# Kernel tuning notes

Hardware: AMD Instinct MI355X
Metric: run time of the kernel (lower is better)

## Reference

```python
import jax, jax.numpy as jnp
import numpy as np

B, N, K, M = 4, 32768, 128, 1024
C_IN, C_OUT, C_ATT, H = 256, 256, 256, 8
G = 32  # GroupNorm groups
EPS = 1e-6


def heat_diffusion(x, mass, evals, evecs, t):
    # to_basis: evecs^T @ (mass * x)  -> [B,K,C]
    x_spec = jnp.einsum('bnk,bnc->bkc', evecs, x * mass[..., None])
    coefs = jnp.exp(-evals[..., None] * t[None, None, :])  # [B,K,C]
    # from_basis: evecs @ spec -> [B,N,C]
    return jnp.einsum('bnk,bkc->bnc', evecs, coefs * x_spec)


def setup_inputs() -> dict:
    key = jax.random.key(0)
    ks = jax.random.split(key, 16)
    x = jax.random.normal(ks[0], (B, N, C_IN), jnp.float32)
    mass = jax.random.uniform(ks[1], (B, N), jnp.float32, 0.1, 1.0)
    evals = jnp.sort(jax.random.uniform(ks[2], (B, K), jnp.float32, 0.0, 10.0), axis=-1)
    evecs = jax.random.normal(ks[3], (B, N, K), jnp.float32) / np.sqrt(N)
    # unique sorted farthest-point indices per mesh (equiv. to boolean mask with M True)
    far_idx = jnp.stack([jnp.sort(jax.random.permutation(jax.random.fold_in(ks[4], b), N)[:M])
                         for b in range(B)]).astype(jnp.int32)
    s = 1.0 / np.sqrt(C_IN)
    params = dict(
        diff_in_t=jnp.full((C_IN,), 0.01, jnp.float32),
        diff_out_t=jnp.full((C_OUT,), 0.01, jnp.float32),
        gn_w=jnp.ones((C_IN,), jnp.float32),
        gn_b=jnp.zeros((C_IN,), jnp.float32),
        Wq=jax.random.normal(ks[5], (C_IN, C_ATT), jnp.float32) * s,
        bq=jnp.zeros((C_ATT,), jnp.float32),
        Wk=jax.random.normal(ks[6], (C_IN, C_ATT), jnp.float32) * s,
        bk=jnp.zeros((C_ATT,), jnp.float32),
        Wv=jax.random.normal(ks[7], (C_IN, C_ATT), jnp.float32) * s,
        bv=jnp.zeros((C_ATT,), jnp.float32),
        Wo=jax.random.normal(ks[8], (C_ATT, C_OUT), jnp.float32) * s,
        bo=jnp.zeros((C_OUT,), jnp.float32),
        out_w=jnp.ones((C_OUT,), jnp.float32),
    )
    return dict(x=x, mass=mass, evals=evals, evecs=evecs, far_idx=far_idx, **params)


def reference(x, mass, evals, evecs, far_idx, diff_in_t, diff_out_t, gn_w, gn_b,
              Wq, bq, Wk, bk, Wv, bv, Wo, bo, out_w):
    # clamp (torch does this in-place under no_grad)
    diff_in_t = jnp.maximum(diff_in_t, 1e-8)
    diff_out_t = jnp.maximum(diff_out_t, 1e-8)
    out_w = jnp.maximum(out_w, 1e-8)

    x = heat_diffusion(x, mass, evals, evecs, diff_in_t)  # [B,N,C_IN]

    # masked gather of farthest points -> [B,M,C_IN]
    x_far = jnp.take_along_axis(x, far_idx[..., None], axis=1)

    # GroupNorm over (group-channels, points)
    xg = x_far.reshape(B, M, G, C_IN // G)
    mu = jnp.mean(xg, axis=(1, 3), keepdims=True)
    var = jnp.var(xg, axis=(1, 3), keepdims=True)
    xg = (xg - mu) * jax.lax.rsqrt(var + EPS)
    x_far = xg.reshape(B, M, C_IN) * gn_w + gn_b

    d = C_ATT // H
    q = (x_far @ Wq + bq).reshape(B, M, H, d)
    k = (x_far @ Wk + bk).reshape(B, M, H, d)
    v = (x_far @ Wv + bv).reshape(B, M, H, d)
    scores = jnp.einsum('bqhd,bkhd->bhqk', q, k) / np.sqrt(d)
    attn = jax.nn.softmax(scores, axis=-1)
    x_far = jnp.einsum('bhqk,bkhd->bqhd', attn, v).reshape(B, M, C_ATT)
    x_far = x_far @ Wo + bo  # [B,M,C_OUT]

    # scatter back into zeros at the farthest-point rows
    z = jnp.zeros((B, N, C_OUT), x.dtype)
    z = z.at[jnp.arange(B)[:, None], far_idx].set(x_far)

    out = heat_diffusion(z, mass, evals, evecs, diff_out_t)
    return out * out_w[None, None, :]
```

## Files before the change

### kernel.cpp

```cpp
#include <hip/hip_runtime.h>
#include <hip/hip_bf16.h>


#define Bn 4
#define Nn 32768
#define Kn 128
#define Cn 256
#define Mn 1024
#define Hn 8
#define Dn 32
#define NCH 64
#define MCH 16

typedef _Float16 f16;
typedef _Float16 f16x8 __attribute__((ext_vector_type(8)));
typedef float f32x4 __attribute__((ext_vector_type(4)));
typedef unsigned int u32;
typedef unsigned int u32x4 __attribute__((ext_vector_type(4)));

__device__ __forceinline__ void gload_lds16(const float* g, float* l) {
    __builtin_amdgcn_global_load_lds(
        (const __attribute__((address_space(1))) void*)g,
        (__attribute__((address_space(3))) void*)l, 16, 0, 0);
}

static __device__ __forceinline__ u32 packf16(f16 a, f16 b) {
    union { f16 h[2]; u32 u; } x;
    x.h[0] = a; x.h[1] = b;
    return x.u;
}

__global__ __launch_bounds__(512) void k_tobasis1(
    const float* __restrict__ x, const float* __restrict__ mass,
    const float* __restrict__ evecs, float* __restrict__ part)
{
    const int nch = blockIdx.x, b = blockIdx.z;
    const int n0 = nch * (Nn / NCH);
    const int t = threadIdx.x;
    const int lane = t & 63, w = t >> 6;
    const int lr = lane & 15, lg = lane >> 4;
    const int wm = (w & 1) * 64;
    const int wc = (w >> 1) * 64;

    __shared__ __align__(16) float evS[2][32][128];
    __shared__ __align__(16) float xS[2][32][256];
    __shared__ __align__(16) f16 evT[128][64];
    __shared__ __align__(16) f16 xT[256][64];
    __shared__ __align__(16) float massS[512];

    const size_t rb0 = (size_t)b * Nn + n0;
    const float* ebase = evecs + rb0 * Kn;
    const float* xbase = x + rb0 * Cn;

    f32x4 acc[4][4] = {};

    if (w < 2) gload_lds16(mass + rb0 + w * 256 + lane * 4, massS + w * 256);
#pragma unroll
    for (int ss = 0; ss < 2; ss++) {
        const float* eb = ebase + (size_t)ss * 32 * Kn;
        const float* xb = xbase + (size_t)ss * 32 * Cn;
#pragma unroll
        for (int iw = 0; iw < 2; iw++)
            gload_lds16(eb + (w * 2 + iw) * 256 + lane * 4, &evS[ss][0][0] + (w * 2 + iw) * 256);
#pragma unroll
        for (int iw = 0; iw < 4; iw++)
            gload_lds16(xb + (w * 4 + iw) * 256 + lane * 4, &xS[ss][0][0] + (w * 4 + iw) * 256);
    }

    for (int s = 0; s < 16; s++) {
        const int p = s & 1;
        if (s == 15) { asm volatile("s_waitcnt vmcnt(0)" ::: "memory"); }
        else         { asm volatile("s_waitcnt vmcnt(6)" ::: "memory"); }
        __builtin_amdgcn_sched_barrier(0);
        __builtin_amdgcn_s_barrier();

        {
            const int k = t & 127;
            const int g = t >> 7;
            f16x8 hv, lv;
#pragma unroll
            for (int r = 0; r < 8; r++) {
                const float f = evS[p][g * 8 + r][k];
                const f16 h = (f16)f;
                hv[r] = h;
                lv[r] = (f16)(f - (float)h);
            }
            *(f16x8*)&evT[k][((g) ^ (k & 7)) * 8] = hv;
            *(f16x8*)&evT[k][((4 + g) ^ (k & 7)) * 8] = lv;
        }
        {
            const int c = t & 255;
            const int g2 = t >> 8;
#pragma unroll
            for (int jj = 0; jj < 2; jj++) {
                const int ch = g2 * 2 + jj;
                f16x8 hv, lv;
#pragma unroll
                for (int r = 0; r < 8; r++) {
                    const int n = ch * 8 + r;
                    const float f = xS[p][n][c] * massS[s * 32 + n];
                    const f16 h = (f16)f;
                    hv[r] = h;
                    lv[r] = (f16)(f - (float)h);
                }
                *(f16x8*)&xT[c][((ch) ^ (c & 7)) * 8] = hv;
                *(f16x8*)&xT[c][((4 + ch) ^ (c & 7)) * 8] = lv;
            }
        }

        asm volatile("s_waitcnt lgkmcnt(0)" ::: "memory");
        __builtin_amdgcn_sched_barrier(0);
        __builtin_amdgcn_s_barrier();

        if (s + 2 < 16) {
            const float* eb = ebase + (size_t)(s + 2) * 32 * Kn;
            const float* xb = xbase + (size_t)(s + 2) * 32 * Cn;
#pragma unroll
            for (int iw = 0; iw < 2; iw++)
                gload_lds16(eb + (w * 2 + iw) * 256 + lane * 4, &evS[p][0][0] + (w * 2 + iw) * 256);
#pragma unroll
            for (int iw = 0; iw < 4; iw++)
                gload_lds16(xb + (w * 4 + iw) * 256 + lane * 4, &xS[p][0][0] + (w * 4 + iw) * 256);
        }

        f16x8 aH[4], aL[4], bH[4], bL[4];
#pragma unroll
        for (int i = 0; i < 4; i++) {
            const int rk = wm + i * 16 + lr;
            aH[i] = *(const f16x8*)&evT[rk][((lg) ^ (rk & 7)) * 8];
            aL[i] = *(const f16x8*)&evT[rk][((4 + lg) ^ (rk & 7)) * 8];
            const int rc = wc + i * 16 + lr;
            bH[i] = *(const f16x8*)&xT[rc][((lg) ^ (rc & 7)) * 8];
            bL[i] = *(const f16x8*)&xT[rc][((4 + lg) ^ (rc & 7)) * 8];
        }
#pragma unroll
        for (int i = 0; i < 4; i++)
#pragma unroll
            for (int j = 0; j < 4; j++) {
                acc[i][j] = __builtin_amdgcn_mfma_f32_16x16x32_f16(aH[i], bH[j], acc[i][j], 0, 0, 0);
                acc[i][j] = __builtin_amdgcn_mfma_f32_16x16x32_f16(aH[i], bL[j], acc[i][j], 0, 0, 0);
                acc[i][j] = __builtin_amdgcn_mfma_f32_16x16x32_f16(aL[i], bH[j], acc[i][j], 0, 0, 0);
            }
    }

    float* dst = part + ((size_t)b * NCH + nch) * (Kn * Cn);
#pragma unroll
    for (int i = 0; i < 4; i++)
#pragma unroll
        for (int j = 0; j < 4; j++) {
            const int m0 = wm + i * 16 + lg * 4;
            const int c = wc + j * 16 + lr;
#pragma unroll
            for (int r = 0; r < 4; r++)
                dst[(size_t)(m0 + r) * Cn + c] = acc[i][j][r];
        }
}

__global__ __launch_bounds__(256) void k_reduce(
    const float* __restrict__ part, int nchunks,
    const float* __restrict__ evals, const float* __restrict__ tvec,
    float* __restrict__ spec)
{
    const int b = blockIdx.x >> 7, k = blockIdx.x & 127, c = threadIdx.x;
    float ssum = 0.f;
    const float* p = part + ((size_t)b * nchunks * Kn + k) * Cn + c;
    for (int j = 0; j < nchunks; j++) ssum += p[(size_t)j * Kn * Cn];
    const float lam = evals[b * Kn + k];
    const float tt = fmaxf(tvec[c], 1e-8f);
    spec[((size_t)b * Kn + k) * Cn + c] = ssum * __expf(-lam * tt);
}

__global__ __launch_bounds__(128) void k_gather(
    const float* __restrict__ evecs, const float* __restrict__ mass,
    const int* __restrict__ far, float* __restrict__ evf, float* __restrict__ massf)
{
    const int row = blockIdx.x;
    const int b = row >> 10;
    const int idx = far[row];
    const int t = threadIdx.x;
    evf[(size_t)row * Kn + t] = evecs[((size_t)b * Nn + idx) * Kn + t];
    if (t == 0) massf[row] = mass[(size_t)b * Nn + idx];
}

struct G3 {
    const float* W[3];
    const float* bias[3];
    float* out[3];
};

template<int KD, bool PERB, bool MMASS>
__global__ __launch_bounds__(256) void k_gemm64(
    const float* __restrict__ X, G3 g, const float* __restrict__ massf)
{
    const int mt = blockIdx.x, ct = blockIdx.y, z = blockIdx.z;
    const int row0 = mt * 64, c0 = ct * 64;
    const int b = row0 >> 10;
    const float* Wp = g.W[z];
    const float* bias = g.bias[z];
    float* out = g.out[z];
    const size_t woff = PERB ? (size_t)b * KD * 256 : 0;

    __shared__ float xT[32][68];
    __shared__ float wl[32][64];
    const int t = threadIdx.x, tx = t & 15, ty = t >> 4;
    float acc[4][4] = {};

    for (int k0 = 0; k0 < KD; k0 += 32) {
        {
            const int m = t >> 2, cc0 = (t & 3) * 8;
            const float* xs = X + (size_t)(row0 + m) * KD + k0 + cc0;
            float4 a0 = *(const float4*)xs, a1 = *(const float4*)(xs + 4);
            xT[cc0 + 0][m] = a0.x; xT[cc0 + 1][m] = a0.y; xT[cc0 + 2][m] = a0.z; xT[cc0 + 3][m] = a0.w;
            xT[cc0 + 4][m] = a1.x; xT[cc0 + 5][m] = a1.y; xT[cc0 + 6][m] = a1.z; xT[cc0 + 7][m] = a1.w;
        }
        {
            const int cc = t >> 3, col = (t & 7) * 8;
            const float* wsrc = Wp + woff + (size_t)(k0 + cc) * 256 + c0 + col;
            float4 a0 = *(const float4*)wsrc, a1 = *(const float4*)(wsrc + 4);
            wl[cc][col + 0] = a0.x; wl[cc][col + 1] = a0.y; wl[cc][col + 2] = a0.z; wl[cc][col + 3] = a0.w;
            wl[cc][col + 4] = a1.x; wl[cc][col + 5] = a1.y; wl[cc][col + 6] = a1.z; wl[cc][col + 7] = a1.w;
        }
        __syncthreads();
#pragma unroll 8
        for (int cc = 0; cc < 32; cc++) {
            float4 xv = *(const float4*)&xT[cc][ty * 4];
            float4 wv = *(const float4*)&wl[cc][tx * 4];
            float xa[4] = {xv.x, xv.y, xv.z, xv.w};
            float wa[4] = {wv.x, wv.y, wv.z, wv.w};
#pragma unroll
            for (int i = 0; i < 4; i++)
#pragma unroll
                for (int j = 0; j < 4; j++) acc[i][j] += xa[i] * wa[j];
        }
        __syncthreads();
    }
    float bj[4] = {0.f, 0.f, 0.f, 0.f};
    if (bias) {
#pragma unroll
        for (int j = 0; j < 4; j++) bj[j] = bias[c0 + tx * 4 + j];
    }
#pragma unroll
    for (int i = 0; i < 4; i++) {
        const int row = row0 + ty * 4 + i;
        const float mm = MMASS ? massf[row] : 1.f;
        *(float4*)(out + (size_t)row * 256 + c0 + tx * 4) =
            make_float4((acc[i][0] + bj[0]) * mm, (acc[i][1] + bj[1]) * mm,
                        (acc[i][2] + bj[2]) * mm, (acc[i][3] + bj[3]) * mm);
    }
}

__global__ __launch_bounds__(256) void k_gnstats(const float* __restrict__ xfar, float* __restrict__ gst)
{
    const int b = blockIdx.x >> 5, g = blockIdx.x & 31;
    const int t = threadIdx.x;
    float s = 0.f, s2 = 0.f;
#pragma unroll
    for (int i = 0; i < 4; i++) {
        const int m = t * 4 + i;
        const float* p = xfar + ((size_t)b * Mn + m) * Cn + g * 8;
        float4 a = *(const float4*)p;
        float4 c = *(const float4*)(p + 4);
        s += a.x + a.y + a.z + a.w + c.x + c.y + c.z + c.w;
        s2 += a.x * a.x + a.y * a.y + a.z * a.z + a.w * a.w +
              c.x * c.x + c.y * c.y + c.z * c.z + c.w * c.w;
    }
    __shared__ float sb[256], sb2[256];
    sb[t] = s; sb2[t] = s2;
    __syncthreads();
    for (int o = 128; o > 0; o >>= 1) {
        if (t < o) { sb[t] += sb[t + o]; sb2[t] += sb2[t + o]; }
        __syncthreads();
    }
    if (t == 0) {
        const float mean = sb[0] * (1.f / 8192.f);
        const float var = sb2[0] * (1.f / 8192.f) - mean * mean;
        gst[2 * blockIdx.x] = mean;
        gst[2 * blockIdx.x + 1] = rsqrtf(var + 1e-6f);
    }
}

__global__ __launch_bounds__(256) void k_gnapply(
    const float* __restrict__ xfar, const float* __restrict__ gst,
    const float* __restrict__ gw, const float* __restrict__ gb, float* __restrict__ xn)
{
    const int idx = (blockIdx.x * 256 + threadIdx.x) * 4;
    const int c = idx & 255;
    const int row = idx >> 8;
    const int b = row >> 10;
    const int g = c >> 3;
    const float2 st = *(const float2*)&gst[2 * (b * 32 + g)];
    float4 vv = *(const float4*)&xfar[idx];
    float4 w4 = *(const float4*)&gw[c];
    float4 b4 = *(const float4*)&gb[c];
    float4 o;
    o.x = (vv.x - st.x) * st.y * w4.x + b4.x;
    o.y = (vv.y - st.x) * st.y * w4.y + b4.y;
    o.z = (vv.z - st.x) * st.y * w4.z + b4.z;
    o.w = (vv.w - st.x) * st.y * w4.w + b4.w;
    *(float4*)&xn[idx] = o;
}

__global__ __launch_bounds__(256) void k_attn(
    const float* __restrict__ q, const float* __restrict__ kbuf, const float* __restrict__ vbuf,
    float* __restrict__ att)
{
    const int qt = blockIdx.x;
    const int bh = blockIdx.y;
    const int b = bh >> 3, h = bh & 7;
    const int t = threadIdx.x;
    const int lane = t & 63, w = t >> 6;
    const int lr = lane & 15, lg = lane >> 4;

    __shared__ __align__(16) f16 Kh[64][32];
    __shared__ __align__(16) f16 Kl[64][32];
    __shared__ __align__(16) f16 Vh[32][64];
    __shared__ __align__(16) f16 Vl[32][64];
    __shared__ __align__(16) u32 Pw[4][16][68];

    const size_t base = (size_t)b * Mn * Cn + h * Dn;
    const int q0 = qt * 64;

    f16x8 Qh, Ql;
    {
        const float* qp = q + base + (size_t)(q0 + w * 16 + lr) * Cn + lg * 8;
        f32x4 a0 = *(const f32x4*)qp;
        f32x4 a1 = *(const f32x4*)(qp + 4);
        const float scale = 0.17677669529663687f;
        float qv[8] = {a0[0], a0[1], a0[2], a0[3], a1[0], a1[1], a1[2], a1[3]};
#pragma unroll
        for (int r = 0; r < 8; r++) {
            const float f = qv[r] * scale;
            const f16 hh = (f16)f;
            Qh[r] = hh;
            Ql[r] = (f16)(f - (float)hh);
        }
    }

    const int krow = t >> 2, kdg = (t & 3) * 8;
    const int vrow = (t & 31) * 2, vdc = (t >> 5) * 4;

    f32x4 kr0, kr1, va, vb;
    {
        const float* kp = kbuf + base + (size_t)krow * Cn + kdg;
        kr0 = *(const f32x4*)kp; kr1 = *(const f32x4*)(kp + 4);
        const float* vp = vbuf + base + (size_t)vrow * Cn + vdc;
        va = *(const f32x4*)vp; vb = *(const f32x4*)(vp + Cn);
    }

    float m_i[4], l_i[4];
    f32x4 acc[2] = {};
#pragma unroll
    for (int r = 0; r < 4; r++) { m_i[r] = -1e30f; l_i[r] = 0.f; }

#pragma unroll 1
    for (int kt = 0; kt < 16; kt++) {
        asm volatile("" ::: "memory");
        __builtin_amdgcn_s_barrier();

        {
            float kv[8] = {kr0[0], kr0[1], kr0[2], kr0[3], kr1[0], kr1[1], kr1[2], kr1[3]};
            f16x8 hv, lv;
#pragma unroll
            for (int r = 0; r < 8; r++) {
                const f16 hh = (f16)kv[r];
                hv[r] = hh;
                lv[r] = (f16)(kv[r] - (float)hh);
            }
            *(f16x8*)&Kh[krow][kdg] = hv;
            *(f16x8*)&Kl[krow][kdg] = lv;
        }
        {
            float v0[4] = {va[0], va[1], va[2], va[3]};
            float v1[4] = {vb[0], vb[1], vb[2], vb[3]};
#pragma unroll
            for (int j = 0; j < 4; j++) {
                const int d = vdc + j;
                const f16 h0 = (f16)v0[j], h1 = (f16)v1[j];
                const f16 l0 = (f16)(v0[j] - (float)h0), l1 = (f16)(v1[j] - (float)h1);
                const int col = vrow >> 1;
                const int idx = (((col >> 2) ^ (d & 7)) << 2) | (col & 3);
                ((u32*)&Vh[d][0])[idx] = packf16(h0, h1);
                ((u32*)&Vl[d][0])[idx] = packf16(l0, l1);
            }
        }
        if (kt < 15) {
            const float* kp = kbuf + base + (size_t)((kt + 1) * 64 + krow) * Cn + kdg;
            kr0 = *(const f32x4*)kp; kr1 = *(const f32x4*)(kp + 4);
            const float* vp = vbuf + base + (size_t)((kt + 1) * 64 + vrow) * Cn + vdc;
            va = *(const f32x4*)vp; vb = *(const f32x4*)(vp + Cn);
        }

        asm volatile("s_waitcnt lgkmcnt(0)" ::: "memory");
        __builtin_amdgcn_sched_barrier(0);
        __builtin_amdgcn_s_barrier();

        f32x4 s[4];
#pragma unroll
        for (int ct = 0; ct < 4; ct++) {
            const f16x8 khi = *(const f16x8*)&Kh[ct * 16 + lr][lg * 8];
            const f16x8 klo = *(const f16x8*)&Kl[ct * 16 + lr][lg * 8];
            f32x4 z = {};
            z = __builtin_amdgcn_mfma_f32_16x16x32_f16(Qh, khi, z, 0, 0, 0);
            z = __builtin_amdgcn_mfma_f32_16x16x32_f16(Qh, klo, z, 0, 0, 0);
            z = __builtin_amdgcn_mfma_f32_16x16x32_f16(Ql, khi, z, 0, 0, 0);
            s[ct] = z;
        }

        float tm[4];
#pragma unroll
        for (int r = 0; r < 4; r++)
            tm[r] = fmaxf(fmaxf(s[0][r], s[1][r]), fmaxf(s[2][r], s[3][r]));
#pragma unroll
        for (int r = 0; r < 4; r++) {
            tm[r] = fmaxf(tm[r], __shfl_xor(tm[r], 1));
            tm[r] = fmaxf(tm[r], __shfl_xor(tm[r], 2));
            tm[r] = fmaxf(tm[r], __shfl_xor(tm[r], 4));
            tm[r] = fmaxf(tm[r], __shfl_xor(tm[r], 8));
        }
        float corr[4], rs[4];
#pragma unroll
        for (int r = 0; r < 4; r++) {
            const float nm = fmaxf(m_i[r], tm[r]);
            corr[r] = __expf(m_i[r] - nm);
            m_i[r] = nm;
            rs[r] = 0.f;
        }
#pragma unroll
        for (int ct = 0; ct < 4; ct++)
#pragma unroll
            for (int r = 0; r < 4; r++) {
                const float p = __expf(s[ct][r] - m_i[r]);
                rs[r] += p;
                const f16 ph = (f16)p;
                const f16 pl = (f16)(p - (float)ph);
                Pw[w][lg * 4 + r][ct * 16 + lr] = packf16(ph, pl);
            }
#pragma unroll
        for (int r = 0; r < 4; r++) {
            rs[r] += __shfl_xor(rs[r], 1);
            rs[r] += __shfl_xor(rs[r], 2);
            rs[r] += __shfl_xor(rs[r], 4);
            rs[r] += __shfl_xor(rs[r], 8);
            l_i[r] = l_i[r] * corr[r] + rs[r];
        }
#pragma unroll
        for (int dt = 0; dt < 2; dt++)
#pragma unroll
            for (int r = 0; r < 4; r++) acc[dt][r] *= corr[r];

        asm volatile("s_waitcnt lgkmcnt(0)" ::: "memory");
        __builtin_amdgcn_sched_barrier(0);

        f16x8 pah[2], pal[2];
#pragma unroll
        for (int kc = 0; kc < 2; kc++) {
            const u32* prow = &Pw[w][lr][0] + kc * 32 + lg * 8;
            u32x4 ua = *(const u32x4*)prow;
            u32x4 ub = *(const u32x4*)(prow + 4);
            union { u32 wd[4]; f16x8 v; } hh, ll;
            hh.wd[0] = __builtin_amdgcn_perm(ua[1], ua[0], 0x05040100u);
            hh.wd[1] = __builtin_amdgcn_perm(ua[3], ua[2], 0x05040100u);
            hh.wd[2] = __builtin_amdgcn_perm(ub[1], ub[0], 0x05040100u);
            hh.wd[3] = __builtin_amdgcn_perm(ub[3], ub[2], 0x05040100u);
            ll.wd[0] = __builtin_amdgcn_perm(ua[1], ua[0], 0x07060302u);
            ll.wd[1] = __builtin_amdgcn_perm(ua[3], ua[2], 0x07060302u);
            ll.wd[2] = __builtin_amdgcn_perm(ub[1], ub[0], 0x07060302u);
            ll.wd[3] = __builtin_amdgcn_perm(ub[3], ub[2], 0x07060302u);
            pah[kc] = hh.v;
            pal[kc] = ll.v;
        }

#pragma unroll
        for (int dt = 0; dt < 2; dt++)
#pragma unroll
            for (int kc = 0; kc < 2; kc++) {
                const int d = dt * 16 + lr;
                const int ch = ((kc * 4 + lg) ^ (lr & 7)) * 8;
                const f16x8 vh = *(const f16x8*)&Vh[d][ch];
                const f16x8 vl = *(const f16x8*)&Vl[d][ch];
                acc[dt] = __builtin_amdgcn_mfma_f32_16x16x32_f16(pah[kc], vh, acc[dt], 0, 0, 0);
                acc[dt] = __builtin_amdgcn_mfma_f32_16x16x32_f16(pah[kc], vl, acc[dt], 0, 0, 0);
                acc[dt] = __builtin_amdgcn_mfma_f32_16x16x32_f16(pal[kc], vh, acc[dt], 0, 0, 0);
            }
    }

#pragma unroll
    for (int r = 0; r < 4; r++) {
        const float inv = 1.f / l_i[r];
        const size_t orow = (size_t)b * Mn + q0 + w * 16 + lg * 4 + r;
#pragma unroll
        for (int dt = 0; dt < 2; dt++)
            att[orow * Cn + h * Dn + dt * 16 + lr] = acc[dt][r] * inv;
    }
}

__global__ __launch_bounds__(256) void k_tobasis2(
    const float* __restrict__ evf, const float* __restrict__ xo, float* __restrict__ part)
{
    const int mch = blockIdx.x, ct = blockIdx.y, b = blockIdx.z;
    const int m0 = mch * (Mn / MCH);
    const int c0 = ct * 128;
    __shared__ float ev[32][128];
    __shared__ float xm[32][128];
    const int t = threadIdx.x, tx = t & 15, ty = t >> 4;
    float acc[8][8];
#pragma unroll
    for (int i = 0; i < 8; i++)
#pragma unroll
        for (int j = 0; j < 8; j++) acc[i][j] = 0.f;
    const int lr = t >> 3, lc = (t & 7) * 16;
    for (int s = 0; s < Mn / MCH; s += 32) {
        const size_t mrow = (size_t)b * Mn + m0 + s + lr;
        {
            const float* es = evf + mrow * Kn + lc;
            *(float4*)&ev[lr][lc]      = *(const float4*)es;
            *(float4*)&ev[lr][lc + 4]  = *(const float4*)(es + 4);
            *(float4*)&ev[lr][lc + 8]  = *(const float4*)(es + 8);
            *(float4*)&ev[lr][lc + 12] = *(const float4*)(es + 12);
            const float* xs = xo + mrow * Cn + c0 + lc;
            *(float4*)&xm[lr][lc]      = *(const float4*)xs;
            *(float4*)&xm[lr][lc + 4]  = *(const float4*)(xs + 4);
            *(float4*)&xm[lr][lc + 8]  = *(const float4*)(xs + 8);
            *(float4*)&xm[lr][lc + 12] = *(const float4*)(xs + 12);
        }
        __syncthreads();
#pragma unroll 4
        for (int nn = 0; nn < 32; nn++) {
            float4 e0 = *(const float4*)&ev[nn][ty * 4];
            float4 e1 = *(const float4*)&ev[nn][64 + ty * 4];
            float4 x0 = *(const float4*)&xm[nn][tx * 4];
            float4 x1 = *(const float4*)&xm[nn][64 + tx * 4];
            float ee[8] = {e0.x, e0.y, e0.z, e0.w, e1.x, e1.y, e1.z, e1.w};
            float xx[8] = {x0.x, x0.y, x0.z, x0.w, x1.x, x1.y, x1.z, x1.w};
#pragma unroll
            for (int i = 0; i < 8; i++)
#pragma unroll
                for (int j = 0; j < 8; j++) acc[i][j] += ee[i] * xx[j];
        }
        __syncthreads();
    }
    float* dst = part + ((size_t)b * MCH + mch) * (Kn * Cn);
#pragma unroll
    for (int i = 0; i < 8; i++) {
        const int k = (i < 4) ? (ty * 4 + i) : (64 + ty * 4 + i - 4);
        *(float4*)(dst + (size_t)k * Cn + c0 + tx * 4) =
            make_float4(acc[i][0], acc[i][1], acc[i][2], acc[i][3]);
        *(float4*)(dst + (size_t)k * Cn + c0 + 64 + tx * 4) =
            make_float4(acc[i][4], acc[i][5], acc[i][6], acc[i][7]);
    }
}

__global__ __launch_bounds__(256) void k_frombasis2(
    const float* __restrict__ evecs, const float* __restrict__ spec,
    const float* __restrict__ outw, float* __restrict__ out)
{
    const int nt = blockIdx.x, ct = blockIdx.y, b = blockIdx.z;
    const int n0 = nt * 128, c0 = ct * 128;
    __shared__ float evT[32][132];
    __shared__ float sp[32][128];
    const int t = threadIdx.x, tx = t & 15, ty = t >> 4;
    float acc[8][8];
#pragma unroll
    for (int i = 0; i < 8; i++)
#pragma unroll
        for (int j = 0; j < 8; j++) acc[i][j] = 0.f;
    const int en = t >> 1, ek0 = (t & 1) * 16;
    const int sr = t >> 3, sc = (t & 7) * 16;
    for (int k0 = 0; k0 < Kn; k0 += 32) {
        {
            const float* es = evecs + ((size_t)b * Nn + n0 + en) * Kn + k0 + ek0;
            float4 a0 = *(const float4*)es, a1 = *(const float4*)(es + 4);
            float4 a2 = *(const float4*)(es + 8), a3 = *(const float4*)(es + 12);
            evT[ek0 + 0][en] = a0.x; evT[ek0 + 1][en] = a0.y; evT[ek0 + 2][en] = a0.z; evT[ek0 + 3][en] = a0.w;
            evT[ek0 + 4][en] = a1.x; evT[ek0 + 5][en] = a1.y; evT[ek0 + 6][en] = a1.z; evT[ek0 + 7][en] = a1.w;
            evT[ek0 + 8][en] = a2.x; evT[ek0 + 9][en] = a2.y; evT[ek0 + 10][en] = a2.z; evT[ek0 + 11][en] = a2.w;
            evT[ek0 + 12][en] = a3.x; evT[ek0 + 13][en] = a3.y; evT[ek0 + 14][en] = a3.z; evT[ek0 + 15][en] = a3.w;
            const float* ss = spec + ((size_t)b * Kn + k0 + sr) * Cn + c0 + sc;
            *(float4*)&sp[sr][sc]      = *(const float4*)ss;
            *(float4*)&sp[sr][sc + 4]  = *(const float4*)(ss + 4);
            *(float4*)&sp[sr][sc + 8]  = *(const float4*)(ss + 8);
            *(float4*)&sp[sr][sc + 12] = *(const float4*)(ss + 12);
        }
        __syncthreads();
#pragma unroll 4
        for (int kk2 = 0; kk2 < 32; kk2++) {
            float4 e0 = *(const float4*)&evT[kk2][ty * 4];
            float4 e1 = *(const float4*)&evT[kk2][64 + ty * 4];
            float4 s0 = *(const float4*)&sp[kk2][tx * 4];
            float4 s1 = *(const float4*)&sp[kk2][64 + tx * 4];
            float ee[8] = {e0.x, e0.y, e0.z, e0.w, e1.x, e1.y, e1.z, e1.w};
            float sv[8] = {s0.x, s0.y, s0.z, s0.w, s1.x, s1.y, s1.z, s1.w};
#pragma unroll
            for (int i = 0; i < 8; i++)
#pragma unroll
                for (int j = 0; j < 8; j++) acc[i][j] += ee[i] * sv[j];
        }
        __syncthreads();
    }
    float ow[8];
#pragma unroll
    for (int j = 0; j < 8; j++) {
        const int c = c0 + ((j < 4) ? (tx * 4 + j) : (64 + tx * 4 + j - 4));
        ow[j] = fmaxf(outw[c], 1e-8f);
    }
#pragma unroll
    for (int i = 0; i < 8; i++) {
        const int n = n0 + ((i < 4) ? (ty * 4 + i) : (64 + ty * 4 + i - 4));
        float* od = out + ((size_t)b * Nn + n) * Cn + c0;
        *(float4*)(od + tx * 4) =
            make_float4(acc[i][0] * ow[0], acc[i][1] * ow[1], acc[i][2] * ow[2], acc[i][3] * ow[3]);
        *(float4*)(od + 64 + tx * 4) =
            make_float4(acc[i][4] * ow[4], acc[i][5] * ow[5], acc[i][6] * ow[6], acc[i][7] * ow[7]);
    }
}

extern "C" void kernel_launch(void* const* d_in, const int* in_sizes, int n_in,
                              void* d_out, int out_size, void* d_ws, size_t ws_size,
                              hipStream_t stream)
{
    const float* x     = (const float*)d_in[0];
    const float* mass  = (const float*)d_in[1];
    const float* evals = (const float*)d_in[2];
    const float* evecs = (const float*)d_in[3];
    const int*   far   = (const int*)d_in[4];
    const float* t_in  = (const float*)d_in[5];
    const float* t_out = (const float*)d_in[6];
    const float* gn_w  = (const float*)d_in[7];
    const float* gn_b  = (const float*)d_in[8];
    const float* Wq    = (const float*)d_in[9];
    const float* bq    = (const float*)d_in[10];
    const float* Wk    = (const float*)d_in[11];
    const float* bk    = (const float*)d_in[12];
    const float* Wv    = (const float*)d_in[13];
    const float* bv    = (const float*)d_in[14];
    const float* Wo    = (const float*)d_in[15];
    const float* bo    = (const float*)d_in[16];
    const float* outw  = (const float*)d_in[17];
    float* out = (float*)d_out;
    float* ws = (float*)d_ws;

    float* A     = ws;
    float* evf   = ws    + 8388608;
    float* massf = evf   + 524288;
    float* gst   = massf + 4096;
    float* pm    = gst   + 256;
    float* pl    = pm    + 262144;
    float* spec1 = pl    + 262144;
    float* xfar  = spec1 + 131072;
    float* xn    = xfar  + 1048576;
    float* q     = xn    + 1048576;
    float* kk    = q     + 1048576;
    float* v     = kk    + 1048576;
    float* part2 = A;
    float* spec2 = spec1;
    float* xo    = xfar;
    float* att   = xn;
    (void)pm; (void)pl;

    k_tobasis1<<<dim3(NCH, 1, Bn), 512, 0, stream>>>(x, mass, evecs, A);
    k_reduce<<<Bn * Kn, Cn, 0, stream>>>(A, NCH, evals, t_in, spec1);
    k_gather<<<Bn * Mn, Kn, 0, stream>>>(evecs, mass, far, evf, massf);
    {
        G3 g{};
        g.W[0] = spec1; g.bias[0] = nullptr; g.out[0] = xfar;
        k_gemm64<128, true, false><<<dim3(64, 4, 1), 256, 0, stream>>>(evf, g, nullptr);
    }
    k_gnstats<<<Bn * 32, 256, 0, stream>>>(xfar, gst);
    k_gnapply<<<1024, 256, 0, stream>>>(xfar, gst, gn_w, gn_b, xn);
    {
        G3 g{};
        g.W[0] = Wq; g.W[1] = Wk; g.W[2] = Wv;
        g.bias[0] = bq; g.bias[1] = bk; g.bias[2] = bv;
        g.out[0] = q; g.out[1] = kk; g.out[2] = v;
        k_gemm64<256, false, false><<<dim3(64, 4, 3), 256, 0, stream>>>(xn, g, nullptr);
    }
    k_attn<<<dim3(16, 32), 256, 0, stream>>>(q, kk, v, att);
    {
        G3 g{};
        g.W[0] = Wo; g.bias[0] = bo; g.out[0] = xo;
        k_gemm64<256, false, true><<<dim3(64, 4, 1), 256, 0, stream>>>(att, g, massf);
    }
    k_tobasis2<<<dim3(MCH, 2, Bn), 256, 0, stream>>>(evf, xo, part2);
    k_reduce<<<Bn * Kn, Cn, 0, stream>>>(part2, MCH, evals, t_out, spec2);
    k_frombasis2<<<dim3(256, 2, Bn), 256, 0, stream>>>(evecs, spec2, outw, out);
}
```

Baseline: 534.9 us.

## Use split-fp16 MFMA for the from-basis GEMM with a transposed spectrum

Replaces the scalar FP32 outer-product from-basis kernel with an MFMA 16x16x32 f16 kernel. Each FP32 operand is split into high and low f16 parts, and three MFMAs per tile keep roughly FP32 accuracy. A new small kernel splits the spectrum and transposes it to a per-channel layout. The evecs are scaled by 256 before the split to avoid f16 underflow, then unscaled in the epilogue. Each block now covers all 256 channels, which removes the duplicate evecs reads. The cost is three MFMAs per product, an extra launch, and some accuracy risk from the split.

```diff
diff --git a/kernel.cpp b/kernel.cpp
--- a/kernel.cpp
+++ b/kernel.cpp
@@ -168,6 +168,35 @@
     const float lam = evals[b * Kn + k];
     const float tt = fmaxf(tvec[c], 1e-8f);
     spec[((size_t)b * Kn + k) * Cn + c] = ssum * __expf(-lam * tt);
+}
+
+__global__ __launch_bounds__(256) void k_spectr(
+    const float* __restrict__ spec, f16* __restrict__ sTh, f16* __restrict__ sTl)
+{
+    const int kc = blockIdx.x, b = blockIdx.y;
+    const int t = threadIdx.x;
+    __shared__ f16 lh[32][258];
+    __shared__ f16 ll[32][258];
+#pragma unroll 8
+    for (int k2 = 0; k2 < 32; k2++) {
+        const float f = spec[((size_t)b * Kn + kc * 32 + k2) * Cn + t];
+        const f16 h = (f16)f;
+        lh[k2][t] = h;
+        ll[k2][t] = (f16)(f - (float)h);
+    }
+    __syncthreads();
+    f16x8 vh[4], vl[4];
+#pragma unroll
+    for (int q = 0; q < 4; q++)
+#pragma unroll
+        for (int j = 0; j < 8; j++) { vh[q][j] = lh[q * 8 + j][t]; vl[q][j] = ll[q * 8 + j][t]; }
+    f16* dh = sTh + ((size_t)b * 256 + t) * Kn + kc * 32;
+    f16* dl = sTl + ((size_t)b * 256 + t) * Kn + kc * 32;
+#pragma unroll
+    for (int q = 0; q < 4; q++) {
+        *(f16x8*)(dh + q * 8) = vh[q];
+        *(f16x8*)(dl + q * 8) = vl[q];
+    }
 }
 
 __global__ __launch_bounds__(128) void k_gather(
@@ -550,68 +579,70 @@
     }
 }
 
-__global__ __launch_bounds__(256) void k_frombasis2(
-    const float* __restrict__ evecs, const float* __restrict__ spec,
-    const float* __restrict__ outw, float* __restrict__ out)
-{
-    const int nt = blockIdx.x, ct = blockIdx.y, b = blockIdx.z;
-    const int n0 = nt * 128, c0 = ct * 128;
-    __shared__ float evT[32][132];
-    __shared__ float sp[32][128];
-    const int t = threadIdx.x, tx = t & 15, ty = t >> 4;
-    float acc[8][8];
-#pragma unroll
-    for (int i = 0; i < 8; i++)
-#pragma unroll
-        for (int j = 0; j < 8; j++) acc[i][j] = 0.f;
-    const int en = t >> 1, ek0 = (t & 1) * 16;
-    const int sr = t >> 3, sc = (t & 7) * 16;
-    for (int k0 = 0; k0 < Kn; k0 += 32) {
-        {
-            const float* es = evecs + ((size_t)b * Nn + n0 + en) * Kn + k0 + ek0;
-            float4 a0 = *(const float4*)es, a1 = *(const float4*)(es + 4);
-            float4 a2 = *(const float4*)(es + 8), a3 = *(const float4*)(es + 12);
-            evT[ek0 + 0][en] = a0.x; evT[ek0 + 1][en] = a0.y; evT[ek0 + 2][en] = a0.z; evT[ek0 + 3][en] = a0.w;
-            evT[ek0 + 4][en] = a1.x; evT[ek0 + 5][en] = a1.y; evT[ek0 + 6][en] = a1.z; evT[ek0 + 7][en] = a1.w;
-            evT[ek0 + 8][en] = a2.x; evT[ek0 + 9][en] = a2.y; evT[ek0 + 10][en] = a2.z; evT[ek0 + 11][en] = a2.w;
-            evT[ek0 + 12][en] = a3.x; evT[ek0 + 13][en] = a3.y; evT[ek0 + 14][en] = a3.z; evT[ek0 + 15][en] = a3.w;
-            const float* ss = spec + ((size_t)b * Kn + k0 + sr) * Cn + c0 + sc;
-            *(float4*)&sp[sr][sc]      = *(const float4*)ss;
-            *(float4*)&sp[sr][sc + 4]  = *(const float4*)(ss + 4);
-            *(float4*)&sp[sr][sc + 8]  = *(const float4*)(ss + 8);
-            *(float4*)&sp[sr][sc + 12] = *(const float4*)(ss + 12);
-        }
-        __syncthreads();
-#pragma unroll 4
-        for (int kk2 = 0; kk2 < 32; kk2++) {
-            float4 e0 = *(const float4*)&evT[kk2][ty * 4];
-            float4 e1 = *(const float4*)&evT[kk2][64 + ty * 4];
-            float4 s0 = *(const float4*)&sp[kk2][tx * 4];
-            float4 s1 = *(const float4*)&sp[kk2][64 + tx * 4];
-            float ee[8] = {e0.x, e0.y, e0.z, e0.w, e1.x, e1.y, e1.z, e1.w};
-            float sv[8] = {s0.x, s0.y, s0.z, s0.w, s1.x, s1.y, s1.z, s1.w};
-#pragma unroll
-            for (int i = 0; i < 8; i++)
-#pragma unroll
-                for (int j = 0; j < 8; j++) acc[i][j] += ee[i] * sv[j];
-        }
-        __syncthreads();
-    }
-    float ow[8];
-#pragma unroll
-    for (int j = 0; j < 8; j++) {
-        const int c = c0 + ((j < 4) ? (tx * 4 + j) : (64 + tx * 4 + j - 4));
-        ow[j] = fmaxf(outw[c], 1e-8f);
-    }
-#pragma unroll
-    for (int i = 0; i < 8; i++) {
-        const int n = n0 + ((i < 4) ? (ty * 4 + i) : (64 + ty * 4 + i - 4));
-        float* od = out + ((size_t)b * Nn + n) * Cn + c0;
-        *(float4*)(od + tx * 4) =
-            make_float4(acc[i][0] * ow[0], acc[i][1] * ow[1], acc[i][2] * ow[2], acc[i][3] * ow[3]);
-        *(float4*)(od + 64 + tx * 4) =
-            make_float4(acc[i][4] * ow[4], acc[i][5] * ow[5], acc[i][6] * ow[6], acc[i][7] * ow[7]);
-    }
+__global__ __launch_bounds__(512) void k_frombasis2(
+    const float* __restrict__ evecs, const f16* __restrict__ sTh,
+    const f16* __restrict__ sTl, const float* __restrict__ outw,
+    float* __restrict__ out)
+{
+    const int nt = blockIdx.x, b = blockIdx.z;
+    const int n0 = nt * 128;
+    const int t = threadIdx.x;
+    const int lane = t & 63, w = t >> 6;
+    const int lr = lane & 15, lg = lane >> 4;
+    const int wn = (w & 1) * 64;
+    const int wc = (w >> 1) * 64;
+
+    const float* Abase = evecs + ((size_t)b * Nn + n0 + wn + lr) * Kn + lg * 8;
+    const f16* Bh = sTh + ((size_t)(b * 256 + wc + lr)) * Kn + lg * 8;
+    const f16* Bl = sTl + ((size_t)(b * 256 + wc + lr)) * Kn + lg * 8;
+
+    f32x4 acc[4][4] = {};
+
+#pragma unroll
+    for (int kk = 0; kk < 4; kk++) {
+        f16x8 bh[4], bl[4];
+#pragma unroll
+        for (int cf = 0; cf < 4; cf++) {
+            bh[cf] = *(const f16x8*)(Bh + (size_t)cf * 16 * Kn + kk * 32);
+            bl[cf] = *(const f16x8*)(Bl + (size_t)cf * 16 * Kn + kk * 32);
+        }
+#pragma unroll
+        for (int rf = 0; rf < 4; rf++) {
+            const float* ap = Abase + (size_t)rf * 16 * Kn + kk * 32;
+            f32x4 a0 = *(const f32x4*)ap;
+            f32x4 a1 = *(const f32x4*)(ap + 4);
+            float av[8] = {a0[0], a0[1], a0[2], a0[3], a1[0], a1[1], a1[2], a1[3]};
+            f16x8 ah, al;
+#pragma unroll
+            for (int r = 0; r < 8; r++) {
+                const float f = av[r] * 256.f;
+                const f16 hh = (f16)f;
+                ah[r] = hh;
+                al[r] = (f16)(f - (float)hh);
+            }
+#pragma unroll
+            for (int cf = 0; cf < 4; cf++) {
+                acc[rf][cf] = __builtin_amdgcn_mfma_f32_16x16x32_f16(ah, bh[cf], acc[rf][cf], 0, 0, 0);
+                acc[rf][cf] = __builtin_amdgcn_mfma_f32_16x16x32_f16(ah, bl[cf], acc[rf][cf], 0, 0, 0);
+                acc[rf][cf] = __builtin_amdgcn_mfma_f32_16x16x32_f16(al, bh[cf], acc[rf][cf], 0, 0, 0);
+            }
+        }
+    }
+
+    float ow4[4];
+#pragma unroll
+    for (int cf = 0; cf < 4; cf++)
+        ow4[cf] = fmaxf(outw[wc + cf * 16 + lr], 1e-8f) * (1.f / 256.f);
+#pragma unroll
+    for (int rf = 0; rf < 4; rf++)
+#pragma unroll
+        for (int cf = 0; cf < 4; cf++) {
+            const int nn = n0 + wn + rf * 16 + lg * 4;
+            const int c = wc + cf * 16 + lr;
+#pragma unroll
+            for (int r = 0; r < 4; r++)
+                out[((size_t)b * Nn + nn + r) * Cn + c] = acc[rf][cf][r] * ow4[cf];
+        }
 }
 
 extern "C" void kernel_launch(void* const* d_in, const int* in_sizes, int n_in,
@@ -655,7 +686,9 @@
     float* spec2 = spec1;
     float* xo    = xfar;
     float* att   = xn;
-    (void)pm; (void)pl;
+    f16* specTh  = (f16*)pm;
+    f16* specTl  = specTh + 131072;
+    (void)pl;
 
     k_tobasis1<<<dim3(NCH, 1, Bn), 512, 0, stream>>>(x, mass, evecs, A);
     k_reduce<<<Bn * Kn, Cn, 0, stream>>>(A, NCH, evals, t_in, spec1);
@@ -682,5 +715,6 @@
     }
     k_tobasis2<<<dim3(MCH, 2, Bn), 256, 0, stream>>>(evf, xo, part2);
     k_reduce<<<Bn * Kn, Cn, 0, stream>>>(part2, MCH, evals, t_out, spec2);
-    k_frombasis2<<<dim3(256, 2, Bn), 256, 0, stream>>>(evecs, spec2, outw, out);
-}
+    k_spectr<<<dim3(4, Bn), 256, 0, stream>>>(spec2, specTh, specTl);
+    k_frombasis2<<<dim3(256, 1, Bn), 512, 0, stream>>>(evecs, specTh, specTl, outw, out);
+}
```

After: 533.0 us. About the same (-0.3%).
